# Kernel optimization log

Measured on AMD Instinct MI355X. Metric: run time of the kernel, lower is better.

## Reference

```python
import jax, jax.numpy as jnp
import numpy as np

B, T, F = 128, 512, 64
H, OUT, NUM_LAYERS = 1024, 64, 2


def _lstm_layer(x, W_ih, W_hh, b_ih, b_hh):
    # x: [B, T, Fin]; W_ih: [4H, Fin]; W_hh: [4H, H]; b_*: [4H]
    # PyTorch gate order: i, f, g, o
    Bsz = x.shape[0]
    Hd = W_hh.shape[1]
    # Precompute input contribution for all timesteps: [B, T, 4H]
    xg = jnp.einsum('btf,gf->btg', x, W_ih) + b_ih + b_hh

    def step(carry, xg_t):
        h, c = carry
        g = xg_t + h @ W_hh.T  # [B, 4H]
        i, f, gg, o = jnp.split(g, 4, axis=-1)
        i = jax.nn.sigmoid(i)
        f = jax.nn.sigmoid(f)
        gg = jnp.tanh(gg)
        o = jax.nn.sigmoid(o)
        c = f * c + i * gg
        h = o * jnp.tanh(c)
        return (h, c), h

    h0 = jnp.zeros((Bsz, Hd), dtype=x.dtype)
    c0 = jnp.zeros((Bsz, Hd), dtype=x.dtype)
    _, hs = jax.lax.scan(step, (h0, c0), jnp.swapaxes(xg, 0, 1))  # hs: [T, B, H]
    return jnp.swapaxes(hs, 0, 1)  # [B, T, H]


def setup_inputs() -> dict:
    key = jax.random.key(0)
    ks = jax.random.split(key, 12)
    s_in = 1.0 / np.sqrt(H)
    inp = {
        'input_batch': jax.random.normal(ks[0], (B, T, F), dtype=jnp.float32),
        'W_ih0': jax.random.uniform(ks[1], (4 * H, F), minval=-s_in, maxval=s_in),
        'W_hh0': jax.random.uniform(ks[2], (4 * H, H), minval=-s_in, maxval=s_in),
        'b_ih0': jax.random.uniform(ks[3], (4 * H,), minval=-s_in, maxval=s_in),
        'b_hh0': jax.random.uniform(ks[4], (4 * H,), minval=-s_in, maxval=s_in),
        'W_ih1': jax.random.uniform(ks[5], (4 * H, H), minval=-s_in, maxval=s_in),
        'W_hh1': jax.random.uniform(ks[6], (4 * H, H), minval=-s_in, maxval=s_in),
        'b_ih1': jax.random.uniform(ks[7], (4 * H,), minval=-s_in, maxval=s_in),
        'b_hh1': jax.random.uniform(ks[8], (4 * H,), minval=-s_in, maxval=s_in),
        'W_fc': jax.random.uniform(ks[9], (OUT, H), minval=-s_in, maxval=s_in),
        'b_fc': jax.random.uniform(ks[10], (OUT,), minval=-s_in, maxval=s_in),
    }
    return inp


def reference(input_batch, W_ih0, W_hh0, b_ih0, b_hh0, W_ih1, W_hh1, b_ih1, b_hh1, W_fc, b_fc):
    # The per-timestep python loop with carried (h, c) is mathematically a full
    # sequence pass through the stacked LSTM, with the Linear applied at every step.
    h1 = _lstm_layer(input_batch, W_ih0, W_hh0, b_ih0, b_hh0)  # [B, T, H]
    h2 = _lstm_layer(h1, W_ih1, W_hh1, b_ih1, b_hh1)           # [B, T, H]
    preds = jnp.einsum('bth,oh->bto', h2, W_fc) + b_fc          # [B, T, OUT]
    return preds
```

## Files before the change

kernel.cpp:

```cpp
#include <hip/hip_runtime.h>
#include <hip/hip_bf16.h>

typedef __bf16 bf16_t;
typedef bf16_t bf16x8 __attribute__((ext_vector_type(8)));
typedef float f32x4 __attribute__((ext_vector_type(4)));
typedef unsigned long long u64;

#define T_SEQ 512
#define NB 128
#define HID 1024
#define FIN 64
#define HB (NB * HID)
#define NBLK 256
#define DM 32
#define DX 8
#define X1SLOT (4096 * NB)

#define NF0 136
#define NF1 128
#define NFR 64
#define L0_STAGE (NF0 * 64 * 8)
#define L1_STAGE (NFR * 64 * 8)
#define LDS_BYTES 151552

#define F0 0
#define FX 64
#define F1 128
#define SYNC_N 256

__device__ __forceinline__ float sigm_f(float x) { return 1.0f / (1.0f + __expf(-x)); }
__device__ __forceinline__ float tanh_f(float x) { return 2.0f * sigm_f(2.0f * x) - 1.0f; }

__device__ __forceinline__ unsigned ldcnt(const unsigned* p) {
    return __hip_atomic_load(p, __ATOMIC_RELAXED, __HIP_MEMORY_SCOPE_AGENT);
}
__device__ __forceinline__ void stw32(unsigned* p, unsigned v) {
    __hip_atomic_store(p, v, __ATOMIC_RELAXED, __HIP_MEMORY_SCOPE_AGENT);
}
__device__ __forceinline__ void stwf(float* p, float v) {
    __hip_atomic_store(p, v, __ATOMIC_RELAXED, __HIP_MEMORY_SCOPE_AGENT);
}
__device__ __forceinline__ void stw64(u64* p, u64 v) {
    __hip_atomic_store(p, v, __ATOMIC_RELAXED, __HIP_MEMORY_SCOPE_AGENT);
}


__global__ __launch_bounds__(256) void prep_kernel(
    const float* __restrict__ x,
    const float* __restrict__ Wih0, const float* __restrict__ Whh0,
    const float* __restrict__ bih0, const float* __restrict__ bhh0,
    const float* __restrict__ Wih1, const float* __restrict__ Whh1,
    const float* __restrict__ bih1, const float* __restrict__ bhh1,
    const float* __restrict__ Wfc,
    bf16_t* __restrict__ Wf0, bf16_t* __restrict__ Wf1, bf16_t* __restrict__ WfR,
    bf16_t* __restrict__ xswz, bf16_t* __restrict__ Wfcb,
    float* __restrict__ bias0, float* __restrict__ bias1,
    bf16_t* __restrict__ mh0, bf16_t* __restrict__ mh1,
    unsigned* __restrict__ sync)
{
    const unsigned stride = gridDim.x * blockDim.x;
    const unsigned i0 = blockIdx.x * blockDim.x + threadIdx.x;

    for (unsigned i = i0; i < SYNC_N; i += stride) sync[i] = 0u;

    for (unsigned i = i0; i < 64u * NF0 * 64u; i += stride) {
        unsigned g0 = i / (NF0 * 64u), rem = i % (NF0 * 64u);
        unsigned f = rem >> 6, ln = rem & 63u;
        unsigned pc = f >> 2, mt = f & 3u;
        unsigned r = mt * 16u + (ln & 15u);
        unsigned row = (r & 3u) * HID + g0 * 16u + (r >> 2);
        unsigned k0 = pc * 32u + (ln >> 4) * 8u;
        bf16_t* dst = Wf0 + (size_t)i * 8;
#pragma unroll
        for (int e = 0; e < 8; ++e) {
            unsigned k = k0 + e;
            float v = (k < FIN) ? Wih0[(size_t)row * FIN + k]
                                : Whh0[(size_t)row * HID + (k - FIN)];
            dst[e] = (bf16_t)v;
        }
    }
    for (unsigned i = i0; i < 64u * NF1 * 64u; i += stride) {
        unsigned g = i >> 13, rem = i & 8191u;
        unsigned f = rem >> 6, ln = rem & 63u;
        unsigned pc = f >> 2, mt = f & 3u;
        unsigned r = mt * 16u + (ln & 15u);
        unsigned row = (r & 3u) * HID + g * 16u + (r >> 2);
        unsigned k0 = pc * 32u + (ln >> 4) * 8u;
        bf16_t* dst = Wf1 + (size_t)i * 8;
#pragma unroll
        for (int e = 0; e < 8; ++e)
            dst[e] = (bf16_t)Wih1[(size_t)row * HID + k0 + e];
    }
    for (unsigned i = i0; i < 128u * NFR * 64u; i += stride) {
        unsigned g1 = i >> 12, rem = i & 4095u;
        unsigned f = rem >> 6, ln = rem & 63u;
        unsigned pc = f >> 1, mt = f & 1u;
        unsigned r = mt * 16u + (ln & 15u);
        unsigned row = (r & 3u) * HID + g1 * 8u + (r >> 2);
        unsigned k0 = pc * 32u + (ln >> 4) * 8u;
        bf16_t* dst = WfR + (size_t)i * 8;
#pragma unroll
        for (int e = 0; e < 8; ++e)
            dst[e] = (bf16_t)Whh1[(size_t)row * HID + k0 + e];
    }
    for (unsigned i = i0; i < 4194304u; i += stride) {
        unsigned e = i & 7u, unit = i >> 3;
        unsigned lane = unit & 63u, g = unit >> 6;
        unsigned wvv = g & 7u, pt = g >> 3;
        unsigned p = pt & 1u, t = pt >> 1;
        unsigned n = wvv * 16u + (lane & 15u);
        unsigned k = p * 32u + (lane >> 4) * 8u + e;
        xswz[i] = (bf16_t)x[((size_t)n * T_SEQ + t) * FIN + k];
    }
    for (unsigned i = i0; i < 64u * HID; i += stride)
        Wfcb[i] = (bf16_t)Wfc[i];
    for (unsigned i = i0; i < (unsigned)(DM * HB); i += stride) {
        mh0[i] = (bf16_t)0.0f; mh1[i] = (bf16_t)0.0f;
    }
    for (unsigned i = i0; i < 4096u; i += stride) {
        bias0[i] = bih0[i] + bhh0[i];
        bias1[i] = bih1[i] + bhh1[i];
    }
}

__global__ __launch_bounds__(512, 2) void lstm_persist(
    const bf16_t* __restrict__ Wf0, const bf16_t* __restrict__ Wf1,
    const bf16_t* __restrict__ WfR,
    const float* __restrict__ bias0, const float* __restrict__ bias1,
    const bf16_t* __restrict__ xswz,
    bf16_t* __restrict__ mh0, bf16_t* __restrict__ mh1,
    bf16_t* __restrict__ h2buf,
    float* __restrict__ x1r,
    unsigned* __restrict__ sync)
{
    extern __shared__ bf16_t Wl[];
    const int b = blockIdx.x;
    const int tid = threadIdx.x;
    const int wv = tid >> 6;
    const int lane = tid & 63;
    const int q = lane >> 4;
    const int l = lane & 15;

    if (b < 64) {
        const int g0 = b;
        const int mh = wv >> 2, nh = wv & 3;
        const int nt0 = nh * 2, nt1 = nh * 2 + 1;
        for (int c = tid; c < NF0 * 64; c += 512)
            *(bf16x8*)(Wl + (size_t)c * 8) =
                *(const bf16x8*)(Wf0 + ((size_t)g0 * (NF0 * 64) + c) * 8);
        bf16_t* stage = Wl + L0_STAGE;
        float* cl = (float*)(Wl + L0_STAGE + 2048);
        for (int i = tid; i < 16 * NB; i += 512) cl[i] = 0.0f;
        float bj[2][4];
#pragma unroll
        for (int mti = 0; mti < 2; ++mti) {
            const int j = g0 * 16 + (mh * 2 + mti) * 4 + q;
#pragma unroll
            for (int gg = 0; gg < 4; ++gg) bj[mti][gg] = bias0[gg * HID + j];
        }
        __syncthreads();

        for (int t = 0; t < T_SEQ; ++t) {
            f32x4 acc[2][2] = {{{0.f,0.f,0.f,0.f},{0.f,0.f,0.f,0.f}},
                               {{0.f,0.f,0.f,0.f},{0.f,0.f,0.f,0.f}}};
            {
                const bf16_t* X = xswz + (size_t)t * 8192;
#pragma unroll
                for (int p = 0; p < 2; ++p) {
                    bf16x8 av0 = *(const bf16x8*)(Wl + ((size_t)(p * 4 + mh * 2) * 64 + lane) * 8);
                    bf16x8 av1 = *(const bf16x8*)(Wl + ((size_t)(p * 4 + mh * 2 + 1) * 64 + lane) * 8);
                    bf16x8 bv0 = *(const bf16x8*)(X + (((size_t)p * 8 + nt0) * 64 + lane) * 8);
                    bf16x8 bv1 = *(const bf16x8*)(X + (((size_t)p * 8 + nt1) * 64 + lane) * 8);
                    acc[0][0] = __builtin_amdgcn_mfma_f32_16x16x32_bf16(av0, bv0, acc[0][0], 0, 0, 0);
                    acc[0][1] = __builtin_amdgcn_mfma_f32_16x16x32_bf16(av0, bv1, acc[0][1], 0, 0, 0);
                    acc[1][0] = __builtin_amdgcn_mfma_f32_16x16x32_bf16(av1, bv0, acc[1][0], 0, 0, 0);
                    acc[1][1] = __builtin_amdgcn_mfma_f32_16x16x32_bf16(av1, bv1, acc[1][1], 0, 0, 0);
                }
            }
            if (wv == 0) {
                const unsigned tA = (unsigned)t;
                const unsigned tB = (t >= DM) ? (unsigned)(t - (DM - 1)) : 0u;
                for (;;) {
                    bool ok = (ldcnt(&sync[F0 + lane]) >= tA)
                           && (ldcnt(&sync[FX + lane]) >= tB);
                    if (__all(ok)) break;
                    __builtin_amdgcn_s_sleep(1);
                }
            }
            __syncthreads();
            {
                const bf16_t* B = mh0 + (size_t)((t + DM - 1) & (DM - 1)) * HB;
                bf16x8 bb0[16], bb1[16];
#pragma unroll
                for (int i = 0; i < 16; ++i) {
                    bb0[i] = *(const bf16x8*)(B + (((size_t)i * 8 + nt0) * 64 + lane) * 8);
                    bb1[i] = *(const bf16x8*)(B + (((size_t)i * 8 + nt1) * 64 + lane) * 8);
                }
#pragma unroll
                for (int p = 0; p < 32; ++p) {
                    bf16x8 av0 = *(const bf16x8*)(Wl + ((size_t)((2 + p) * 4 + mh * 2) * 64 + lane) * 8);
                    bf16x8 av1 = *(const bf16x8*)(Wl + ((size_t)((2 + p) * 4 + mh * 2 + 1) * 64 + lane) * 8);
                    acc[0][0] = __builtin_amdgcn_mfma_f32_16x16x32_bf16(av0, bb0[p & 15], acc[0][0], 0, 0, 0);
                    acc[0][1] = __builtin_amdgcn_mfma_f32_16x16x32_bf16(av0, bb1[p & 15], acc[0][1], 0, 0, 0);
                    acc[1][0] = __builtin_amdgcn_mfma_f32_16x16x32_bf16(av1, bb0[p & 15], acc[1][0], 0, 0, 0);
                    acc[1][1] = __builtin_amdgcn_mfma_f32_16x16x32_bf16(av1, bb1[p & 15], acc[1][1], 0, 0, 0);
                    if (p + 16 < 32) {
                        bb0[p & 15] = *(const bf16x8*)(B + (((size_t)(p + 16) * 8 + nt0) * 64 + lane) * 8);
                        bb1[p & 15] = *(const bf16x8*)(B + (((size_t)(p + 16) * 8 + nt1) * 64 + lane) * 8);
                    }
                }
            }
#pragma unroll
            for (int mti = 0; mti < 2; ++mti) {
                const int u = (mh * 2 + mti) * 4 + q;
#pragma unroll
                for (int nti = 0; nti < 2; ++nti) {
                    const int n = (nh * 2 + nti) * 16 + l;
                    float iv = sigm_f(acc[mti][nti][0] + bj[mti][0]);
                    float fv = sigm_f(acc[mti][nti][1] + bj[mti][1]);
                    float gv = tanh_f(acc[mti][nti][2] + bj[mti][2]);
                    float ov = sigm_f(acc[mti][nti][3] + bj[mti][3]);
                    float cn = fv * cl[u * NB + n] + iv * gv;
                    cl[u * NB + n] = cn;
                    stage[n * 16 + u] = (bf16_t)(ov * tanh_f(cn));
                }
            }
            __syncthreads();
            if (tid < 256) {
                const int n = tid >> 1, half = tid & 1;
                u64 v0 = *(const u64*)(stage + n * 16 + half * 8);
                u64 v1 = *(const u64*)(stage + n * 16 + half * 8 + 4);
                size_t unit = ((size_t)((g0 >> 1) * 8 + (n >> 4))) * 64
                              + ((g0 & 1) * 2 + half) * 16 + (n & 15);
                u64* dst = (u64*)(mh0 + (size_t)(t & (DM - 1)) * HB) + unit * 2;
                stw64(dst, v0); stw64(dst + 1, v1);
            }
            __syncthreads();
            if (tid == 0) stw32(&sync[F0 + g0], (unsigned)(t + 1));
        }
    } else if (b < 128) {
        const int g = b - 64;
        const int mh = wv >> 2, nh = wv & 3;
        const int nt0 = nh * 2, nt1 = nh * 2 + 1;
        for (int c = tid; c < NF1 * 64; c += 512)
            *(bf16x8*)(Wl + (size_t)c * 8) =
                *(const bf16x8*)(Wf1 + ((size_t)g * (NF1 * 64) + c) * 8);
        __syncthreads();

        for (int t = 0; t < T_SEQ; ++t) {
            if (wv == 0) {
                const unsigned tA = (unsigned)(t + 1);
                const unsigned tC = (t >= DX) ? (unsigned)(t - (DX - 1)) : 0u;
                for (;;) {
                    bool ok = (ldcnt(&sync[F0 + lane]) >= tA)
                           && (ldcnt(&sync[F1 + lane]) >= tC)
                           && (ldcnt(&sync[F1 + 64 + lane]) >= tC);
                    if (__all(ok)) break;
                    __builtin_amdgcn_s_sleep(1);
                }
            }
            __syncthreads();
            f32x4 acc[2][2] = {{{0.f,0.f,0.f,0.f},{0.f,0.f,0.f,0.f}},
                               {{0.f,0.f,0.f,0.f},{0.f,0.f,0.f,0.f}}};
            {
                const bf16_t* B = mh0 + (size_t)(t & (DM - 1)) * HB;
                bf16x8 bb0[16], bb1[16];
#pragma unroll
                for (int i = 0; i < 16; ++i) {
                    bb0[i] = *(const bf16x8*)(B + (((size_t)i * 8 + nt0) * 64 + lane) * 8);
                    bb1[i] = *(const bf16x8*)(B + (((size_t)i * 8 + nt1) * 64 + lane) * 8);
                }
#pragma unroll
                for (int p = 0; p < 32; ++p) {
                    bf16x8 av0 = *(const bf16x8*)(Wl + ((size_t)(p * 4 + mh * 2) * 64 + lane) * 8);
                    bf16x8 av1 = *(const bf16x8*)(Wl + ((size_t)(p * 4 + mh * 2 + 1) * 64 + lane) * 8);
                    acc[0][0] = __builtin_amdgcn_mfma_f32_16x16x32_bf16(av0, bb0[p & 15], acc[0][0], 0, 0, 0);
                    acc[0][1] = __builtin_amdgcn_mfma_f32_16x16x32_bf16(av0, bb1[p & 15], acc[0][1], 0, 0, 0);
                    acc[1][0] = __builtin_amdgcn_mfma_f32_16x16x32_bf16(av1, bb0[p & 15], acc[1][0], 0, 0, 0);
                    acc[1][1] = __builtin_amdgcn_mfma_f32_16x16x32_bf16(av1, bb1[p & 15], acc[1][1], 0, 0, 0);
                    if (p + 16 < 32) {
                        bb0[p & 15] = *(const bf16x8*)(B + (((size_t)(p + 16) * 8 + nt0) * 64 + lane) * 8);
                        bb1[p & 15] = *(const bf16x8*)(B + (((size_t)(p + 16) * 8 + nt1) * 64 + lane) * 8);
                    }
                }
            }
            {
                float* P = x1r + (size_t)(t & (DX - 1)) * X1SLOT + (size_t)g * 64 * NB;
#pragma unroll
                for (int mti = 0; mti < 2; ++mti) {
                    const int u = (mh * 2 + mti) * 4 + q;
#pragma unroll
                    for (int nti = 0; nti < 2; ++nti) {
                        const int n = (nh * 2 + nti) * 16 + l;
#pragma unroll
                        for (int jj = 0; jj < 4; ++jj)
                            stwf(P + (size_t)(u * 4 + jj) * NB + n, acc[mti][nti][jj]);
                    }
                }
            }
            __syncthreads();
            if (tid == 0) stw32(&sync[FX + g], (unsigned)(t + 1));
        }
    } else {
        const int g1 = b - 128;
        const int nn = wv * 16 + l;
        for (int c = tid; c < NFR * 64; c += 512)
            *(bf16x8*)(Wl + (size_t)c * 8) =
                *(const bf16x8*)(WfR + ((size_t)g1 * (NFR * 64) + c) * 8);
        bf16_t* stage = Wl + L1_STAGE;
        float* cl = (float*)(Wl + L1_STAGE + 1024);
        for (int i = tid; i < 8 * NB; i += 512) cl[i] = 0.0f;
        float bj[2][4];
#pragma unroll
        for (int mt = 0; mt < 2; ++mt) {
            const int j = g1 * 8 + mt * 4 + q;
#pragma unroll
            for (int gg = 0; gg < 4; ++gg) bj[mt][gg] = bias1[gg * HID + j];
        }
        __syncthreads();

        for (int t = 0; t < T_SEQ; ++t) {
            if (wv == 0) {
                const unsigned tA = (unsigned)(t + 1);
                const unsigned tO = (unsigned)t;
                const unsigned gx = (unsigned)(g1 >> 1);
                for (;;) {
                    bool ok = (ldcnt(&sync[FX + gx]) >= tA)
                           && (ldcnt(&sync[F1 + lane]) >= tO)
                           && (ldcnt(&sync[F1 + 64 + lane]) >= tO);
                    if (__all(ok)) break;
                    __builtin_amdgcn_s_sleep(1);
                }
            }
            __syncthreads();
            float pv[2][4];
            {
                const float* P = x1r + (size_t)(t & (DX - 1)) * X1SLOT + (size_t)g1 * 32 * NB;
#pragma unroll
                for (int mt = 0; mt < 2; ++mt)
#pragma unroll
                    for (int jj = 0; jj < 4; ++jj)
                        pv[mt][jj] = P[(size_t)((mt * 4 + q) * 4 + jj) * NB + nn];
            }
            f32x4 acc[2] = {{0.f,0.f,0.f,0.f},{0.f,0.f,0.f,0.f}};
            {
                const bf16_t* B1 = mh1 + (size_t)((t + DM - 1) & (DM - 1)) * HB;
                bf16x8 bb[32];
#pragma unroll
                for (int i = 0; i < 32; ++i)
                    bb[i] = *(const bf16x8*)(B1 + (((size_t)i * 8 + wv) * 64 + lane) * 8);
#pragma unroll
                for (int p = 0; p < 32; ++p) {
#pragma unroll
                    for (int mt = 0; mt < 2; ++mt) {
                        bf16x8 av = *(const bf16x8*)(Wl + ((size_t)(p * 2 + mt) * 64 + lane) * 8);
                        acc[mt] = __builtin_amdgcn_mfma_f32_16x16x32_bf16(av, bb[p], acc[mt], 0, 0, 0);
                    }
                }
            }
#pragma unroll
            for (int mt = 0; mt < 2; ++mt) {
                const int u = mt * 4 + q;
                float iv = sigm_f(acc[mt][0] + pv[mt][0] + bj[mt][0]);
                float fv = sigm_f(acc[mt][1] + pv[mt][1] + bj[mt][1]);
                float gv = tanh_f(acc[mt][2] + pv[mt][2] + bj[mt][2]);
                float ov = sigm_f(acc[mt][3] + pv[mt][3] + bj[mt][3]);
                float cn = fv * cl[u * NB + nn] + iv * gv;
                cl[u * NB + nn] = cn;
                stage[nn * 8 + u] = (bf16_t)(ov * tanh_f(cn));
            }
            __asm__ volatile("s_waitcnt lgkmcnt(0)" ::: "memory");
            u64 v = 0;
            if (q < 2) {
                v = *(const u64*)(stage + (size_t)(wv * 16 + l) * 8 + q * 4);
                size_t unit = ((size_t)(g1 >> 2) * 8 + wv) * 64 + (size_t)(g1 & 3) * 16 + l;
                stw64((u64*)(mh1 + (size_t)(t & (DM - 1)) * HB) + unit * 2 + q, v);
            }
            __syncthreads();
            if (tid == 0) stw32(&sync[F1 + g1], (unsigned)(t + 1));
            if (q < 2)
                *(u64*)(h2buf + ((size_t)(wv * 16 + l) * T_SEQ + t) * HID + g1 * 8 + q * 4) = v;
        }
    }
}

__global__ __launch_bounds__(256) void fc_kernel(
    const bf16_t* __restrict__ h2buf, const bf16_t* __restrict__ Wfcb,
    const float* __restrict__ bfc, float* __restrict__ out)
{
    const int tid = threadIdx.x, wv = tid >> 6, lane = tid & 63;
    const int q = lane >> 4, l = lane & 15;
    const int m0 = blockIdx.x * 64 + wv * 16;
    const bf16_t* arow = h2buf + (size_t)(m0 + l) * HID + q * 8;
    const bf16_t* brow = Wfcb + (size_t)l * HID + q * 8;
    f32x4 acc[4] = {{0.f,0.f,0.f,0.f},{0.f,0.f,0.f,0.f},{0.f,0.f,0.f,0.f},{0.f,0.f,0.f,0.f}};
#pragma unroll 4
    for (int p = 0; p < 32; ++p) {
        bf16x8 av = *(const bf16x8*)(arow + p * 32);
#pragma unroll
        for (int ntile = 0; ntile < 4; ++ntile) {
            bf16x8 bv = *(const bf16x8*)(brow + (size_t)ntile * 16 * HID + p * 32);
            acc[ntile] = __builtin_amdgcn_mfma_f32_16x16x32_bf16(av, bv, acc[ntile], 0, 0, 0);
        }
    }
#pragma unroll
    for (int ntile = 0; ntile < 4; ++ntile) {
        float bv = bfc[ntile * 16 + l];
#pragma unroll
        for (int r = 0; r < 4; ++r)
            out[(size_t)(m0 + q * 4 + r) * 64 + ntile * 16 + l] = acc[ntile][r] + bv;
    }
}

extern "C" void kernel_launch(void* const* d_in, const int* in_sizes, int n_in,
                              void* d_out, int out_size, void* d_ws, size_t ws_size,
                              hipStream_t stream)
{
    const float* x    = (const float*)d_in[0];
    const float* Wih0 = (const float*)d_in[1];
    const float* Whh0 = (const float*)d_in[2];
    const float* bih0 = (const float*)d_in[3];
    const float* bhh0 = (const float*)d_in[4];
    const float* Wih1 = (const float*)d_in[5];
    const float* Whh1 = (const float*)d_in[6];
    const float* bih1 = (const float*)d_in[7];
    const float* bhh1 = (const float*)d_in[8];
    const float* Wfc  = (const float*)d_in[9];
    const float* bfc  = (const float*)d_in[10];
    float* out = (float*)d_out;

    char* ws = (char*)d_ws;
    size_t off = 0;
    auto alloc = [&](size_t bytes) -> void* {
        void* p = ws + off;
        off += (bytes + 255) & ~(size_t)255;
        return p;
    };
    bf16_t* Wf0  = (bf16_t*)alloc((size_t)64 * NF0 * 64 * 8 * 2);
    bf16_t* Wf1  = (bf16_t*)alloc((size_t)64 * NF1 * 64 * 8 * 2);
    bf16_t* WfR  = (bf16_t*)alloc((size_t)128 * NFR * 64 * 8 * 2);
    bf16_t* xswz = (bf16_t*)alloc((size_t)NB * T_SEQ * FIN * 2);
    bf16_t* h2buf= (bf16_t*)alloc((size_t)NB * T_SEQ * HID * 2);
    bf16_t* mh0  = (bf16_t*)alloc((size_t)DM * HB * 2);
    bf16_t* mh1  = (bf16_t*)alloc((size_t)DM * HB * 2);
    float*  x1r  = (float*)alloc((size_t)DX * X1SLOT * 4);
    float*  bias0= (float*)alloc(4096 * 4);
    float*  bias1= (float*)alloc(4096 * 4);
    bf16_t* Wfcb = (bf16_t*)alloc((size_t)64 * HID * 2);
    unsigned* syncp = (unsigned*)alloc(SYNC_N * 4);
    if (off > ws_size) return;

    hipFuncSetAttribute((const void*)lstm_persist,
                        hipFuncAttributeMaxDynamicSharedMemorySize, LDS_BYTES);

    prep_kernel<<<1024, 256, 0, stream>>>(x, Wih0, Whh0, bih0, bhh0,
                                          Wih1, Whh1, bih1, bhh1, Wfc,
                                          Wf0, Wf1, WfR, xswz, Wfcb,
                                          bias0, bias1, mh0, mh1, syncp);

    void* args[] = { (void*)&Wf0, (void*)&Wf1, (void*)&WfR,
                     (void*)&bias0, (void*)&bias1,
                     (void*)&xswz, (void*)&mh0, (void*)&mh1,
                     (void*)&h2buf, (void*)&x1r,
                     (void*)&syncp };
    hipLaunchCooperativeKernel((void*)lstm_persist, dim3(NBLK), dim3(512),
                               args, LDS_BYTES, stream);

    fc_kernel<<<(NB * T_SEQ) / 64, 256, 0, stream>>>(h2buf, Wfcb, bfc, out);
}
```

Baseline: 4.774 ms.

## Remap LSTM waves to full M-tiles per batch column and issue all h loads upfront

Layer-0 and layer-1 input blocks now give each wave one 16-column batch tile and all four 16-row gate tiles, replacing the 2x2 split. This halves the global h-vector loads per wave and makes the mapping match the recurrent-tail blocks. All 32 h fragments are issued as inline-asm global_load_dwordx4 up front, with explicit vmcnt waits and sched barriers so the first half of MFMAs overlaps the second half's loads. The cost is more LDS weight reads per wave and higher VGPR pressure, with 32 outstanding 16-byte loads per wave under 2-blocks-per-CU launch bounds.

```diff
diff --git a/kernel.cpp b/kernel.cpp
--- a/kernel.cpp
+++ b/kernel.cpp
@@ -43,6 +43,9 @@
 __device__ __forceinline__ void stw64(u64* p, u64 v) {
     __hip_atomic_store(p, v, __ATOMIC_RELAXED, __HIP_MEMORY_SCOPE_AGENT);
 }
+
+#define GLOAD16(dst, addr) \
+    asm volatile("global_load_dwordx4 %0, %1, off" : "=v"(dst) : "v"(addr))
 
 
 __global__ __launch_bounds__(256) void prep_kernel(
@@ -140,41 +143,37 @@
     const int lane = tid & 63;
     const int q = lane >> 4;
     const int l = lane & 15;
+    const int nn = wv * 16 + l;
 
     if (b < 64) {
         const int g0 = b;
-        const int mh = wv >> 2, nh = wv & 3;
-        const int nt0 = nh * 2, nt1 = nh * 2 + 1;
         for (int c = tid; c < NF0 * 64; c += 512)
             *(bf16x8*)(Wl + (size_t)c * 8) =
                 *(const bf16x8*)(Wf0 + ((size_t)g0 * (NF0 * 64) + c) * 8);
         bf16_t* stage = Wl + L0_STAGE;
         float* cl = (float*)(Wl + L0_STAGE + 2048);
         for (int i = tid; i < 16 * NB; i += 512) cl[i] = 0.0f;
-        float bj[2][4];
-#pragma unroll
-        for (int mti = 0; mti < 2; ++mti) {
-            const int j = g0 * 16 + (mh * 2 + mti) * 4 + q;
-#pragma unroll
-            for (int gg = 0; gg < 4; ++gg) bj[mti][gg] = bias0[gg * HID + j];
+        float bj[4][4];
+#pragma unroll
+        for (int mt = 0; mt < 4; ++mt) {
+            const int j = g0 * 16 + mt * 4 + q;
+#pragma unroll
+            for (int gg = 0; gg < 4; ++gg) bj[mt][gg] = bias0[gg * HID + j];
         }
         __syncthreads();
 
         for (int t = 0; t < T_SEQ; ++t) {
-            f32x4 acc[2][2] = {{{0.f,0.f,0.f,0.f},{0.f,0.f,0.f,0.f}},
-                               {{0.f,0.f,0.f,0.f},{0.f,0.f,0.f,0.f}}};
+            f32x4 acc[4] = {{0.f,0.f,0.f,0.f},{0.f,0.f,0.f,0.f},{0.f,0.f,0.f,0.f},{0.f,0.f,0.f,0.f}};
             {
                 const bf16_t* X = xswz + (size_t)t * 8192;
 #pragma unroll
                 for (int p = 0; p < 2; ++p) {
-                    bf16x8 av0 = *(const bf16x8*)(Wl + ((size_t)(p * 4 + mh * 2) * 64 + lane) * 8);
-                    bf16x8 av1 = *(const bf16x8*)(Wl + ((size_t)(p * 4 + mh * 2 + 1) * 64 + lane) * 8);
-                    bf16x8 bv0 = *(const bf16x8*)(X + (((size_t)p * 8 + nt0) * 64 + lane) * 8);
-                    bf16x8 bv1 = *(const bf16x8*)(X + (((size_t)p * 8 + nt1) * 64 + lane) * 8);
-                    acc[0][0] = __builtin_amdgcn_mfma_f32_16x16x32_bf16(av0, bv0, acc[0][0], 0, 0, 0);
-                    acc[0][1] = __builtin_amdgcn_mfma_f32_16x16x32_bf16(av0, bv1, acc[0][1], 0, 0, 0);
-                    acc[1][0] = __builtin_amdgcn_mfma_f32_16x16x32_bf16(av1, bv0, acc[1][0], 0, 0, 0);
-                    acc[1][1] = __builtin_amdgcn_mfma_f32_16x16x32_bf16(av1, bv1, acc[1][1], 0, 0, 0);
+                    bf16x8 bv = *(const bf16x8*)(X + (((size_t)p * 8 + wv) * 64 + lane) * 8);
+#pragma unroll
+                    for (int mt = 0; mt < 4; ++mt) {
+                        bf16x8 av = *(const bf16x8*)(Wl + ((size_t)(p * 4 + mt) * 64 + lane) * 8);
+                        acc[mt] = __builtin_amdgcn_mfma_f32_16x16x32_bf16(av, bv, acc[mt], 0, 0, 0);
+                    }
                 }
             }
             if (wv == 0) {
@@ -190,40 +189,45 @@
             __syncthreads();
             {
                 const bf16_t* B = mh0 + (size_t)((t + DM - 1) & (DM - 1)) * HB;
-                bf16x8 bb0[16], bb1[16];
-#pragma unroll
-                for (int i = 0; i < 16; ++i) {
-                    bb0[i] = *(const bf16x8*)(B + (((size_t)i * 8 + nt0) * 64 + lane) * 8);
-                    bb1[i] = *(const bf16x8*)(B + (((size_t)i * 8 + nt1) * 64 + lane) * 8);
-                }
-#pragma unroll
-                for (int p = 0; p < 32; ++p) {
-                    bf16x8 av0 = *(const bf16x8*)(Wl + ((size_t)((2 + p) * 4 + mh * 2) * 64 + lane) * 8);
-                    bf16x8 av1 = *(const bf16x8*)(Wl + ((size_t)((2 + p) * 4 + mh * 2 + 1) * 64 + lane) * 8);
-                    acc[0][0] = __builtin_amdgcn_mfma_f32_16x16x32_bf16(av0, bb0[p & 15], acc[0][0], 0, 0, 0);
-                    acc[0][1] = __builtin_amdgcn_mfma_f32_16x16x32_bf16(av0, bb1[p & 15], acc[0][1], 0, 0, 0);
-                    acc[1][0] = __builtin_amdgcn_mfma_f32_16x16x32_bf16(av1, bb0[p & 15], acc[1][0], 0, 0, 0);
-                    acc[1][1] = __builtin_amdgcn_mfma_f32_16x16x32_bf16(av1, bb1[p & 15], acc[1][1], 0, 0, 0);
-                    if (p + 16 < 32) {
-                        bb0[p & 15] = *(const bf16x8*)(B + (((size_t)(p + 16) * 8 + nt0) * 64 + lane) * 8);
-                        bb1[p & 15] = *(const bf16x8*)(B + (((size_t)(p + 16) * 8 + nt1) * 64 + lane) * 8);
-                    }
-                }
-            }
-#pragma unroll
-            for (int mti = 0; mti < 2; ++mti) {
-                const int u = (mh * 2 + mti) * 4 + q;
-#pragma unroll
-                for (int nti = 0; nti < 2; ++nti) {
-                    const int n = (nh * 2 + nti) * 16 + l;
-                    float iv = sigm_f(acc[mti][nti][0] + bj[mti][0]);
-                    float fv = sigm_f(acc[mti][nti][1] + bj[mti][1]);
-                    float gv = tanh_f(acc[mti][nti][2] + bj[mti][2]);
-                    float ov = sigm_f(acc[mti][nti][3] + bj[mti][3]);
-                    float cn = fv * cl[u * NB + n] + iv * gv;
-                    cl[u * NB + n] = cn;
-                    stage[n * 16 + u] = (bf16_t)(ov * tanh_f(cn));
-                }
+                f32x4 bb[32];
+#pragma unroll
+                for (int i = 0; i < 32; ++i) {
+                    const bf16_t* a = B + (((size_t)i * 8 + wv) * 64 + lane) * 8;
+                    GLOAD16(bb[i], a);
+                }
+                asm volatile("s_waitcnt vmcnt(16)" ::: "memory");
+                __builtin_amdgcn_sched_barrier(0);
+#pragma unroll
+                for (int p = 0; p < 16; ++p) {
+                    bf16x8 bv = __builtin_bit_cast(bf16x8, bb[p]);
+#pragma unroll
+                    for (int mt = 0; mt < 4; ++mt) {
+                        bf16x8 av = *(const bf16x8*)(Wl + ((size_t)((2 + p) * 4 + mt) * 64 + lane) * 8);
+                        acc[mt] = __builtin_amdgcn_mfma_f32_16x16x32_bf16(av, bv, acc[mt], 0, 0, 0);
+                    }
+                }
+                asm volatile("s_waitcnt vmcnt(0)" ::: "memory");
+                __builtin_amdgcn_sched_barrier(0);
+#pragma unroll
+                for (int p = 16; p < 32; ++p) {
+                    bf16x8 bv = __builtin_bit_cast(bf16x8, bb[p]);
+#pragma unroll
+                    for (int mt = 0; mt < 4; ++mt) {
+                        bf16x8 av = *(const bf16x8*)(Wl + ((size_t)((2 + p) * 4 + mt) * 64 + lane) * 8);
+                        acc[mt] = __builtin_amdgcn_mfma_f32_16x16x32_bf16(av, bv, acc[mt], 0, 0, 0);
+                    }
+                }
+            }
+#pragma unroll
+            for (int mt = 0; mt < 4; ++mt) {
+                const int u = mt * 4 + q;
+                float iv = sigm_f(acc[mt][0] + bj[mt][0]);
+                float fv = sigm_f(acc[mt][1] + bj[mt][1]);
+                float gv = tanh_f(acc[mt][2] + bj[mt][2]);
+                float ov = sigm_f(acc[mt][3] + bj[mt][3]);
+                float cn = fv * cl[u * NB + nn] + iv * gv;
+                cl[u * NB + nn] = cn;
+                stage[nn * 16 + u] = (bf16_t)(ov * tanh_f(cn));
             }
             __syncthreads();
             if (tid < 256) {
@@ -240,8 +244,6 @@
         }
     } else if (b < 128) {
         const int g = b - 64;
-        const int mh = wv >> 2, nh = wv & 3;
-        const int nt0 = nh * 2, nt1 = nh * 2 + 1;
         for (int c = tid; c < NF1 * 64; c += 512)
             *(bf16x8*)(Wl + (size_t)c * 8) =
                 *(const bf16x8*)(Wf1 + ((size_t)g * (NF1 * 64) + c) * 8);
@@ -260,42 +262,46 @@
                 }
             }
             __syncthreads();
-            f32x4 acc[2][2] = {{{0.f,0.f,0.f,0.f},{0.f,0.f,0.f,0.f}},
-                               {{0.f,0.f,0.f,0.f},{0.f,0.f,0.f,0.f}}};
+            f32x4 acc[4] = {{0.f,0.f,0.f,0.f},{0.f,0.f,0.f,0.f},{0.f,0.f,0.f,0.f},{0.f,0.f,0.f,0.f}};
             {
                 const bf16_t* B = mh0 + (size_t)(t & (DM - 1)) * HB;
-                bf16x8 bb0[16], bb1[16];
-#pragma unroll
-                for (int i = 0; i < 16; ++i) {
-                    bb0[i] = *(const bf16x8*)(B + (((size_t)i * 8 + nt0) * 64 + lane) * 8);
-                    bb1[i] = *(const bf16x8*)(B + (((size_t)i * 8 + nt1) * 64 + lane) * 8);
-                }
-#pragma unroll
-                for (int p = 0; p < 32; ++p) {
-                    bf16x8 av0 = *(const bf16x8*)(Wl + ((size_t)(p * 4 + mh * 2) * 64 + lane) * 8);
-                    bf16x8 av1 = *(const bf16x8*)(Wl + ((size_t)(p * 4 + mh * 2 + 1) * 64 + lane) * 8);
-                    acc[0][0] = __builtin_amdgcn_mfma_f32_16x16x32_bf16(av0, bb0[p & 15], acc[0][0], 0, 0, 0);
-                    acc[0][1] = __builtin_amdgcn_mfma_f32_16x16x32_bf16(av0, bb1[p & 15], acc[0][1], 0, 0, 0);
-                    acc[1][0] = __builtin_amdgcn_mfma_f32_16x16x32_bf16(av1, bb0[p & 15], acc[1][0], 0, 0, 0);
-                    acc[1][1] = __builtin_amdgcn_mfma_f32_16x16x32_bf16(av1, bb1[p & 15], acc[1][1], 0, 0, 0);
-                    if (p + 16 < 32) {
-                        bb0[p & 15] = *(const bf16x8*)(B + (((size_t)(p + 16) * 8 + nt0) * 64 + lane) * 8);
-                        bb1[p & 15] = *(const bf16x8*)(B + (((size_t)(p + 16) * 8 + nt1) * 64 + lane) * 8);
+                f32x4 bb[32];
+#pragma unroll
+                for (int i = 0; i < 32; ++i) {
+                    const bf16_t* a = B + (((size_t)i * 8 + wv) * 64 + lane) * 8;
+                    GLOAD16(bb[i], a);
+                }
+                asm volatile("s_waitcnt vmcnt(16)" ::: "memory");
+                __builtin_amdgcn_sched_barrier(0);
+#pragma unroll
+                for (int p = 0; p < 16; ++p) {
+                    bf16x8 bv = __builtin_bit_cast(bf16x8, bb[p]);
+#pragma unroll
+                    for (int mt = 0; mt < 4; ++mt) {
+                        bf16x8 av = *(const bf16x8*)(Wl + ((size_t)(p * 4 + mt) * 64 + lane) * 8);
+                        acc[mt] = __builtin_amdgcn_mfma_f32_16x16x32_bf16(av, bv, acc[mt], 0, 0, 0);
+                    }
+                }
+                asm volatile("s_waitcnt vmcnt(0)" ::: "memory");
+                __builtin_amdgcn_sched_barrier(0);
+#pragma unroll
+                for (int p = 16; p < 32; ++p) {
+                    bf16x8 bv = __builtin_bit_cast(bf16x8, bb[p]);
+#pragma unroll
+                    for (int mt = 0; mt < 4; ++mt) {
+                        bf16x8 av = *(const bf16x8*)(Wl + ((size_t)(p * 4 + mt) * 64 + lane) * 8);
+                        acc[mt] = __builtin_amdgcn_mfma_f32_16x16x32_bf16(av, bv, acc[mt], 0, 0, 0);
                     }
                 }
             }
             {
                 float* P = x1r + (size_t)(t & (DX - 1)) * X1SLOT + (size_t)g * 64 * NB;
 #pragma unroll
-                for (int mti = 0; mti < 2; ++mti) {
-                    const int u = (mh * 2 + mti) * 4 + q;
-#pragma unroll
-                    for (int nti = 0; nti < 2; ++nti) {
-                        const int n = (nh * 2 + nti) * 16 + l;
-#pragma unroll
-                        for (int jj = 0; jj < 4; ++jj)
-                            stwf(P + (size_t)(u * 4 + jj) * NB + n, acc[mti][nti][jj]);
-                    }
+                for (int mt = 0; mt < 4; ++mt) {
+                    const int u = mt * 4 + q;
+#pragma unroll
+                    for (int jj = 0; jj < 4; ++jj)
+                        stwf(P + (size_t)(u * 4 + jj) * NB + nn, acc[mt][jj]);
                 }
             }
             __syncthreads();
@@ -303,7 +309,6 @@
         }
     } else {
         const int g1 = b - 128;
-        const int nn = wv * 16 + l;
         for (int c = tid; c < NFR * 64; c += 512)
             *(bf16x8*)(Wl + (size_t)c * 8) =
                 *(const bf16x8*)(WfR + ((size_t)g1 * (NFR * 64) + c) * 8);
@@ -345,16 +350,32 @@
             f32x4 acc[2] = {{0.f,0.f,0.f,0.f},{0.f,0.f,0.f,0.f}};
             {
                 const bf16_t* B1 = mh1 + (size_t)((t + DM - 1) & (DM - 1)) * HB;
-                bf16x8 bb[32];
-#pragma unroll
-                for (int i = 0; i < 32; ++i)
-                    bb[i] = *(const bf16x8*)(B1 + (((size_t)i * 8 + wv) * 64 + lane) * 8);
-#pragma unroll
-                for (int p = 0; p < 32; ++p) {
+                f32x4 bb[32];
+#pragma unroll
+                for (int i = 0; i < 32; ++i) {
+                    const bf16_t* a = B1 + (((size_t)i * 8 + wv) * 64 + lane) * 8;
+                    GLOAD16(bb[i], a);
+                }
+                asm volatile("s_waitcnt vmcnt(16)" ::: "memory");
+                __builtin_amdgcn_sched_barrier(0);
+#pragma unroll
+                for (int p = 0; p < 16; ++p) {
+                    bf16x8 bv = __builtin_bit_cast(bf16x8, bb[p]);
 #pragma unroll
                     for (int mt = 0; mt < 2; ++mt) {
                         bf16x8 av = *(const bf16x8*)(Wl + ((size_t)(p * 2 + mt) * 64 + lane) * 8);
-                        acc[mt] = __builtin_amdgcn_mfma_f32_16x16x32_bf16(av, bb[p], acc[mt], 0, 0, 0);
+                        acc[mt] = __builtin_amdgcn_mfma_f32_16x16x32_bf16(av, bv, acc[mt], 0, 0, 0);
+                    }
+                }
+                asm volatile("s_waitcnt vmcnt(0)" ::: "memory");
+                __builtin_amdgcn_sched_barrier(0);
+#pragma unroll
+                for (int p = 16; p < 32; ++p) {
+                    bf16x8 bv = __builtin_bit_cast(bf16x8, bb[p]);
+#pragma unroll
+                    for (int mt = 0; mt < 2; ++mt) {
+                        bf16x8 av = *(const bf16x8*)(Wl + ((size_t)(p * 2 + mt) * 64 + lane) * 8);
+                        acc[mt] = __builtin_amdgcn_mfma_f32_16x16x32_bf16(av, bv, acc[mt], 0, 0, 0);
                     }
                 }
             }
```

Result: slower. 5.000 ms (+4.7%).
